# Kernel tuning notes

Hardware: AMD Instinct MI355X
Metric: run time of the kernel (lower is better)

The kernel has to match this reference:

```python
import jax, jax.numpy as jnp
import numpy as np

B = 128      # trees per batch
D = 10       # tree depth (perfect binary tree)
L = 2 ** D   # leaves per tree
V = 50000    # vocab
E = 300      # embed size
C = 5        # num classes


def setup_inputs() -> dict:
    key = jax.random.key(0)
    k0, k1, k2, k3 = jax.random.split(key, 4)
    return {
        "word_ids": jax.random.randint(k0, (B, L), 0, V),
        "embedding": jax.random.normal(k1, (V, E), jnp.float32) * 0.02,
        "W_w": jax.random.normal(k2, (E, 2 * E), jnp.float32) * (1.0 / np.sqrt(2 * E)),
        "W_b": jnp.zeros((E,), jnp.float32),
        "P_w": jax.random.normal(k3, (C, E), jnp.float32) * (1.0 / np.sqrt(E)),
        "P_b": jnp.zeros((C,), jnp.float32),
    }


def reference(word_ids, embedding, W_w, W_b, P_w, P_b):
    # Leaf nodes: relu(Embedding(word))  -> [B, L, E]
    h = jax.nn.relu(embedding[word_ids])
    # projection of every node (torch Linear: x @ W.T + b)
    logits = [jnp.einsum("bne,ce->bnc", h, P_w) + P_b]
    # Combine same-depth sibling pairs level by level (D fixed levels).
    for _ in range(D):
        pair = jnp.concatenate([h[:, 0::2], h[:, 1::2]], axis=-1)  # [B, n/2, 2E]
        h = jax.nn.relu(jnp.einsum("bnf,ef->bne", pair, W_w) + W_b)  # [B, n/2, E]
        logits.append(jnp.einsum("bne,ce->bnc", h, P_w) + P_b)
    # All node logits, leaves first then each internal level up to the root.
    return jnp.concatenate(logits, axis=1)  # [B, 2L-1, C]
```

## Files before the change

kernel.cpp:

```cpp
#include <hip/hip_runtime.h>
#include <hip/hip_bf16.h>

#define B_ 128
#define D_ 10
#define L_ 1024
#define E_ 300
#define C_ 5
#define NODES 2047
#define HSTR 304
#define KP 608
#define NP 320
#define PK 320
#define LSTR 328

typedef __attribute__((ext_vector_type(8))) short short8;
typedef __attribute__((ext_vector_type(4))) float f32x4;
typedef __hip_bfloat16 bf16;

__device__ __forceinline__ short f2bs(float v) {
  bf16 b = (bf16)v;
  return *reinterpret_cast<short*>(&b);
}

__device__ __forceinline__ short8 pack_relu(f32x4 v0, f32x4 v1) {
  short8 s;
#pragma unroll
  for (int j = 0; j < 4; j++) s[j] = f2bs(fmaxf(v0[j], 0.f));
#pragma unroll
  for (int j = 0; j < 4; j++) s[4 + j] = f2bs(fmaxf(v1[j], 0.f));
  return s;
}

__global__ __launch_bounds__(256) void prep_k(
    const float* __restrict__ emb, const float* __restrict__ Ww,
    const float* __restrict__ Pw, bf16* __restrict__ T, bf16* __restrict__ Wp,
    bf16* __restrict__ Pp, bf16* __restrict__ Pq, int V) {
  int idx = blockIdx.x * 256 + threadIdx.x;
  int tchunks = V * 38;
  if (idx < tchunks) {
    int v = idx / 38, c = idx % 38;
    const float* src = emb + (size_t)v * E_ + c * 8;
    f32x4 v0 = *(const f32x4*)src;
    f32x4 v1;
    if (c == 37) v1 = (f32x4){0.f, 0.f, 0.f, 0.f};
    else v1 = *(const f32x4*)(src + 4);
    *(short8*)(T + (size_t)v * HSTR + c * 8) = pack_relu(v0, v1);
  }
  if (idx < NP * KP) {
    int r = idx / KP, c = idx % KP;
    float v = 0.f;
    if (r < E_) {
      if (c < E_) v = Ww[r * 600 + c];
      else if (c >= HSTR && c < HSTR + E_) v = Ww[r * 600 + (c - 4)];
    }
    Wp[idx] = (bf16)v;
  }
  if (idx < 16 * PK) {
    int r = idx / PK, c = idx % PK;
    float v = (r < C_ && c < E_) ? Pw[r * E_ + c] : 0.f;
    Pp[idx] = (bf16)v;
  }
  if (idx < 2 * 16 * KP) {
    int p = idx / (16 * KP);
    int rem = idx % (16 * KP);
    int r = rem / KP, c = rem % KP;
    int e = c - p * HSTR;
    float v = (r < C_ && e >= 0 && e < E_) ? Pw[r * E_ + e] : 0.f;
    Pq[idx] = (bf16)v;
  }
}

__global__ __launch_bounds__(256) void fused_l1_k(
    const int* __restrict__ wid, const bf16* __restrict__ T,
    const bf16* __restrict__ Wp, const float* __restrict__ Wb,
    const bf16* __restrict__ Pq, const bf16* __restrict__ Pp,
    const float* __restrict__ Pb, bf16* __restrict__ h1,
    float* __restrict__ out) {
  __shared__ bf16 hs[64][LSTR];
  int tid = threadIdx.x;
  int w = tid >> 6, l = tid & 63, q = l & 15, half = l >> 4;
  int m0 = blockIdx.x * 64;

  int off0[4], off1[4];
#pragma unroll
  for (int rt = 0; rt < 4; rt++) {
    int mrow = m0 + rt * 16 + q;
    off0[rt] = wid[2 * mrow] * HSTR;
    off1[rt] = wid[2 * mrow + 1] * HSTR;
  }
  int lm = m0 + w * 16 + q;
  int lb0 = wid[2 * lm] * HSTR;
  int lb1 = wid[2 * lm + 1] * HSTR;

  f32x4 acc[4][5];
#pragma unroll
  for (int rt = 0; rt < 4; rt++)
#pragma unroll
    for (int nt = 0; nt < 5; nt++) acc[rt][nt] = (f32x4){0.f, 0.f, 0.f, 0.f};
  f32x4 pacc[2];
  pacc[0] = pacc[1] = (f32x4){0.f, 0.f, 0.f, 0.f};

  for (int ks = 0; ks < 19; ks++) {
    int k0 = ks * 32 + half * 8;
    int sel = k0 >= HSTR;
    int e0 = sel ? k0 - HSTR : k0;
    short8 a[4];
#pragma unroll
    for (int rt = 0; rt < 4; rt++)
      a[rt] = *(const short8*)(T + (sel ? off1[rt] : off0[rt]) + e0);
    short8 al = *(const short8*)(T + (sel ? lb1 : lb0) + e0);
    short8 pq0 = *(const short8*)(Pq + (size_t)q * KP + k0);
    short8 pq1 = *(const short8*)(Pq + (size_t)(16 + q) * KP + k0);
    pacc[0] = __builtin_amdgcn_mfma_f32_16x16x32_bf16(al, pq0, pacc[0], 0, 0, 0);
    pacc[1] = __builtin_amdgcn_mfma_f32_16x16x32_bf16(al, pq1, pacc[1], 0, 0, 0);
#pragma unroll
    for (int nt = 0; nt < 5; nt++) {
      short8 b =
          *(const short8*)(Wp + (size_t)(w * 80 + nt * 16 + q) * KP + k0);
#pragma unroll
      for (int rt = 0; rt < 4; rt++)
        acc[rt][nt] = __builtin_amdgcn_mfma_f32_16x16x32_bf16(a[rt], b,
                                                              acc[rt][nt], 0,
                                                              0, 0);
    }
  }

#pragma unroll
  for (int nt = 0; nt < 5; nt++) {
    int n = w * 80 + nt * 16 + q;
    float wb = (n < E_) ? Wb[n] : 0.f;
#pragma unroll
    for (int rt = 0; rt < 4; rt++)
#pragma unroll
      for (int j = 0; j < 4; j++) {
        int rl = rt * 16 + half * 4 + j;
        hs[rl][n] = (bf16)fmaxf(acc[rt][nt][j] + wb, 0.f);
      }
  }
  if (q < C_) {
    float pb = Pb[q];
#pragma unroll
    for (int p = 0; p < 2; p++)
#pragma unroll
      for (int j = 0; j < 4; j++) {
        int leaf = 2 * (m0 + w * 16 + half * 4 + j) + p;
        out[((size_t)(leaf >> 10) * NODES + (leaf & 1023)) * C_ + q] =
            pacc[p][j] + pb;
      }
  }
  __syncthreads();

  for (int i = tid; i < 64 * 38; i += 256) {
    int r = i / 38, c = i % 38;
    *(short8*)(h1 + (size_t)(m0 + r) * HSTR + c * 8) =
        *(const short8*)&hs[r][c * 8];
  }
  f32x4 pc = (f32x4){0.f, 0.f, 0.f, 0.f};
#pragma unroll
  for (int ks = 0; ks < 10; ks++) {
    int k0 = ks * 32 + half * 8;
    short8 a = *(const short8*)&hs[16 * w + q][k0];
    short8 b = *(const short8*)(Pp + (size_t)q * PK + k0);
    pc = __builtin_amdgcn_mfma_f32_16x16x32_bf16(a, b, pc, 0, 0, 0);
  }
  if (q < C_) {
    float pb = Pb[q];
#pragma unroll
    for (int j = 0; j < 4; j++) {
      int m = m0 + w * 16 + half * 4 + j;
      out[((size_t)(m >> 9) * NODES + 1024 + (m & 511)) * C_ + q] = pc[j] + pb;
    }
  }
}

__global__ __launch_bounds__(256) void combine_mfma_k(
    const bf16* __restrict__ h_in, const bf16* __restrict__ Wp,
    const float* __restrict__ Wb, const bf16* __restrict__ Pp,
    const float* __restrict__ Pb, bf16* __restrict__ h_out,
    float* __restrict__ out, int node_off, int nshift) {
  __shared__ bf16 hs[64][LSTR];
  int tid = threadIdx.x;
  int w = tid >> 6;
  int l = tid & 63;
  int q = l & 15;
  int half = l >> 4;
  size_t m0 = (size_t)blockIdx.x * 64;

  f32x4 acc[4][5];
#pragma unroll
  for (int rt = 0; rt < 4; rt++)
#pragma unroll
    for (int nt = 0; nt < 5; nt++) acc[rt][nt] = (f32x4){0.f, 0.f, 0.f, 0.f};

#pragma unroll 2
  for (int ks = 0; ks < 19; ks++) {
    int k0 = ks * 32 + half * 8;
    short8 a[4], b[5];
#pragma unroll
    for (int rt = 0; rt < 4; rt++)
      a[rt] = *(const short8*)(h_in + (m0 + rt * 16 + q) * KP + k0);
#pragma unroll
    for (int nt = 0; nt < 5; nt++)
      b[nt] = *(const short8*)(Wp + (size_t)(w * 80 + nt * 16 + q) * KP + k0);
#pragma unroll
    for (int rt = 0; rt < 4; rt++)
#pragma unroll
      for (int nt = 0; nt < 5; nt++)
        acc[rt][nt] = __builtin_amdgcn_mfma_f32_16x16x32_bf16(
            a[rt], b[nt], acc[rt][nt], 0, 0, 0);
  }

  float wb[5];
#pragma unroll
  for (int nt = 0; nt < 5; nt++) {
    int n = w * 80 + nt * 16 + q;
    wb[nt] = (n < E_) ? Wb[n] : 0.f;
  }
#pragma unroll
  for (int rt = 0; rt < 4; rt++)
#pragma unroll
    for (int nt = 0; nt < 5; nt++) {
      int n = w * 80 + nt * 16 + q;
#pragma unroll
      for (int j = 0; j < 4; j++) {
        int rl = rt * 16 + half * 4 + j;
        hs[rl][n] = (bf16)fmaxf(acc[rt][nt][j] + wb[nt], 0.f);
      }
    }
  __syncthreads();

  for (int i = tid; i < 64 * 38; i += 256) {
    int r = i / 38, c = i % 38;
    *(short8*)(h_out + (m0 + r) * HSTR + c * 8) = *(const short8*)&hs[r][c * 8];
  }

  f32x4 pacc = (f32x4){0.f, 0.f, 0.f, 0.f};
#pragma unroll
  for (int ks = 0; ks < 10; ks++) {
    short8 a = *(const short8*)(&hs[16 * w + q][ks * 32 + half * 8]);
    short8 b = *(const short8*)(Pp + (size_t)q * PK + ks * 32 + half * 8);
    pacc = __builtin_amdgcn_mfma_f32_16x16x32_bf16(a, b, pacc, 0, 0, 0);
  }
  if (q < C_) {
    float pb = Pb[q];
#pragma unroll
    for (int j = 0; j < 4; j++) {
      size_t m = m0 + w * 16 + half * 4 + j;
      size_t b_ = m >> nshift;
      size_t n = m & (((size_t)1 << nshift) - 1);
      out[((size_t)b_ * NODES + node_off + n) * C_ + q] = pacc[j] + pb;
    }
  }
}

__global__ __launch_bounds__(256) void tail_k(
    const bf16* __restrict__ h5, const bf16* __restrict__ Wp,
    const float* __restrict__ Wb, const bf16* __restrict__ Pp,
    const float* __restrict__ Pb, float* __restrict__ out) {
  __shared__ bf16 bufs[2][32][LSTR];
  int tid = threadIdx.x, b = blockIdx.x;
  int w = tid >> 6, l = tid & 63, q = l & 15, half = l >> 4;

  for (int i = tid; i < 32 * 38; i += 256) {
    int r = i / 38, c = i % 38;
    *(short8*)&bufs[0][r][c * 8] =
        *(const short8*)(h5 + ((size_t)b * 32 + r) * HSTR + c * 8);
  }
  __syncthreads();

  int p = 0, off = 2016, Mo = 16;
  for (int lev = 0; lev < 5; lev++) {
    f32x4 acc[5];
#pragma unroll
    for (int t = 0; t < 5; t++) acc[t] = (f32x4){0.f, 0.f, 0.f, 0.f};
    for (int ks = 0; ks < 19; ks++) {
      int k0 = ks * 32 + half * 8;
      int sel = k0 >= HSTR;
      int e0 = k0 - (sel ? HSTR : 0);
      short8 a = *(const short8*)&bufs[p][2 * q + sel][e0];
#pragma unroll
      for (int t = 0; t < 5; t++) {
        int nt = w + 4 * t;
        short8 bfr = *(const short8*)(Wp + ((size_t)nt * 16 + q) * KP + k0);
        acc[t] =
            __builtin_amdgcn_mfma_f32_16x16x32_bf16(a, bfr, acc[t], 0, 0, 0);
      }
    }
    __syncthreads();
#pragma unroll
    for (int t = 0; t < 5; t++) {
      int nt = w + 4 * t;
      int n = nt * 16 + q;
      float wb = (n < E_) ? Wb[n] : 0.f;
#pragma unroll
      for (int j = 0; j < 4; j++) {
        int r = half * 4 + j;
        bufs[p ^ 1][r][n] = (bf16)fmaxf(acc[t][j] + wb, 0.f);
      }
    }
    __syncthreads();
    if (w == 0) {
      f32x4 pc = (f32x4){0.f, 0.f, 0.f, 0.f};
#pragma unroll
      for (int ks = 0; ks < 10; ks++) {
        int k0 = ks * 32 + half * 8;
        short8 a = *(const short8*)&bufs[p ^ 1][q][k0];
        short8 bfr = *(const short8*)(Pp + (size_t)q * PK + k0);
        pc = __builtin_amdgcn_mfma_f32_16x16x32_bf16(a, bfr, pc, 0, 0, 0);
      }
      if (q < C_) {
        float pb = Pb[q];
#pragma unroll
        for (int j = 0; j < 4; j++) {
          int r = half * 4 + j;
          if (r < Mo) out[((size_t)b * NODES + off + r) * C_ + q] = pc[j] + pb;
        }
      }
    }
    p ^= 1;
    off += Mo;
    Mo >>= 1;
  }
}

extern "C" void kernel_launch(void* const* d_in, const int* in_sizes, int n_in,
                              void* d_out, int out_size, void* d_ws,
                              size_t ws_size, hipStream_t stream) {
  const int* wid = (const int*)d_in[0];
  const float* emb = (const float*)d_in[1];
  const float* Ww = (const float*)d_in[2];
  const float* Wb = (const float*)d_in[3];
  const float* Pw = (const float*)d_in[4];
  const float* Pb = (const float*)d_in[5];
  float* out = (float*)d_out;
  int V = in_sizes[1] / E_;

  bf16* hA = (bf16*)d_ws;
  bf16* hB = hA + (size_t)B_ * 512 * HSTR;
  bf16* Wp = hB + (size_t)B_ * 256 * HSTR;
  bf16* Pp = Wp + (size_t)NP * KP;
  bf16* Pq = Pp + (size_t)16 * PK;
  bf16* T = Pq + (size_t)2 * 16 * KP;

  int tchunks = V * 38;
  prep_k<<<(tchunks + 255) / 256, 256, 0, stream>>>(emb, Ww, Pw, T, Wp, Pp, Pq,
                                                    V);
  fused_l1_k<<<(B_ * 512) / 64, 256, 0, stream>>>(wid, T, Wp, Wb, Pq, Pp, Pb,
                                                  hA, out);
  bf16* cur = hA;
  int node_off = 1536;
  for (int lev = 2; lev <= 5; lev++) {
    int n_half = L_ >> lev;
    int M = B_ * n_half;
    bf16* nxt = (lev & 1) ? hA : hB;
    combine_mfma_k<<<M / 64, 256, 0, stream>>>(cur, Wp, Wb, Pp, Pb, nxt, out,
                                               node_off, D_ - lev);
    node_off += n_half;
    cur = nxt;
  }
  tail_k<<<B_, 256, 0, stream>>>(cur, Wp, Wb, Pp, Pb, out);
}
```

Measured before the change: 211.4 us.

## Shrink row tiles per block, add occupancy bounds and software-pipelined gather loads

Each block in the level-1 and combine kernels now covers fewer rows (32 or 16 instead of 64), so more blocks launch for the small later levels. LDS use shrinks and launch bounds request 4 blocks per CU, aiming at higher occupancy. The level-1 embedding gather is prefetched two k-steps ahead to hide load latency. The leaf projection is split across waves, and the tail of the projection K loop is zero-masked. In exchange, each W tile is reused across fewer rows, so there is more global/L2 traffic per output and a risk of register spills.

```diff
diff --git a/kernel.cpp b/kernel.cpp
--- a/kernel.cpp
+++ b/kernel.cpp
@@ -70,185 +70,193 @@
   }
 }
 
-__global__ __launch_bounds__(256) void fused_l1_k(
+#define PROJ_A(rowptr, ks, k0)                                        \
+  ((ks) == 9 && half >= 2 ? (short8){0, 0, 0, 0, 0, 0, 0, 0}          \
+                          : *(const short8*)((rowptr) + (k0)))
+
+__global__ __launch_bounds__(256, 4) void fused_l1_k(
     const int* __restrict__ wid, const bf16* __restrict__ T,
     const bf16* __restrict__ Wp, const float* __restrict__ Wb,
     const bf16* __restrict__ Pq, const bf16* __restrict__ Pp,
     const float* __restrict__ Pb, bf16* __restrict__ h1,
     float* __restrict__ out) {
-  __shared__ bf16 hs[64][LSTR];
+  __shared__ bf16 hs[33][HSTR];
   int tid = threadIdx.x;
   int w = tid >> 6, l = tid & 63, q = l & 15, half = l >> 4;
-  int m0 = blockIdx.x * 64;
-
-  int off0[4], off1[4];
-#pragma unroll
-  for (int rt = 0; rt < 4; rt++) {
-    int mrow = m0 + rt * 16 + q;
-    off0[rt] = wid[2 * mrow] * HSTR;
-    off1[rt] = wid[2 * mrow + 1] * HSTR;
-  }
-  int lm = m0 + w * 16 + q;
-  int lb0 = wid[2 * lm] * HSTR;
-  int lb1 = wid[2 * lm + 1] * HSTR;
-
-  f32x4 acc[4][5];
-#pragma unroll
-  for (int rt = 0; rt < 4; rt++)
+  int m0 = blockIdx.x * 32;
+
+  int mr0 = m0 + q, mr1 = m0 + 16 + q;
+  int o0a = wid[2 * mr0] * HSTR, o0b = wid[2 * mr0 + 1] * HSTR;
+  int o1a = wid[2 * mr1] * HSTR, o1b = wid[2 * mr1 + 1] * HSTR;
+
+  int p = w & 1, rtl = w >> 1;
+
+  f32x4 acc[2][5];
+#pragma unroll
+  for (int rt = 0; rt < 2; rt++)
 #pragma unroll
     for (int nt = 0; nt < 5; nt++) acc[rt][nt] = (f32x4){0.f, 0.f, 0.f, 0.f};
-  f32x4 pacc[2];
-  pacc[0] = pacc[1] = (f32x4){0.f, 0.f, 0.f, 0.f};
+  f32x4 pacc = (f32x4){0.f, 0.f, 0.f, 0.f};
+
+#define LDA(ks, d0, d1)                                          \
+  {                                                              \
+    int k0_ = (ks) * 32 + half * 8;                              \
+    int sel_ = k0_ >= HSTR;                                      \
+    int e0_ = sel_ ? k0_ - HSTR : k0_;                           \
+    d0 = *(const short8*)(T + (sel_ ? o0b : o0a) + e0_);         \
+    d1 = *(const short8*)(T + (sel_ ? o1b : o1a) + e0_);         \
+  }
+
+  short8 aA0, aA1, aB0, aB1, aC0, aC1;
+  LDA(0, aA0, aA1);
+  LDA(1, aB0, aB1);
 
   for (int ks = 0; ks < 19; ks++) {
+    int kn = ks + 2 <= 18 ? ks + 2 : 18;
+    LDA(kn, aC0, aC1);
     int k0 = ks * 32 + half * 8;
-    int sel = k0 >= HSTR;
-    int e0 = sel ? k0 - HSTR : k0;
-    short8 a[4];
-#pragma unroll
-    for (int rt = 0; rt < 4; rt++)
-      a[rt] = *(const short8*)(T + (sel ? off1[rt] : off0[rt]) + e0);
-    short8 al = *(const short8*)(T + (sel ? lb1 : lb0) + e0);
-    short8 pq0 = *(const short8*)(Pq + (size_t)q * KP + k0);
-    short8 pq1 = *(const short8*)(Pq + (size_t)(16 + q) * KP + k0);
-    pacc[0] = __builtin_amdgcn_mfma_f32_16x16x32_bf16(al, pq0, pacc[0], 0, 0, 0);
-    pacc[1] = __builtin_amdgcn_mfma_f32_16x16x32_bf16(al, pq1, pacc[1], 0, 0, 0);
+    short8 al = rtl ? aA1 : aA0;
+    short8 pqf = *(const short8*)(Pq + ((size_t)p * 16 + q) * KP + k0);
+    pacc = __builtin_amdgcn_mfma_f32_16x16x32_bf16(al, pqf, pacc, 0, 0, 0);
 #pragma unroll
     for (int nt = 0; nt < 5; nt++) {
       short8 b =
           *(const short8*)(Wp + (size_t)(w * 80 + nt * 16 + q) * KP + k0);
-#pragma unroll
-      for (int rt = 0; rt < 4; rt++)
-        acc[rt][nt] = __builtin_amdgcn_mfma_f32_16x16x32_bf16(a[rt], b,
-                                                              acc[rt][nt], 0,
-                                                              0, 0);
-    }
-  }
+      acc[0][nt] =
+          __builtin_amdgcn_mfma_f32_16x16x32_bf16(aA0, b, acc[0][nt], 0, 0, 0);
+      acc[1][nt] =
+          __builtin_amdgcn_mfma_f32_16x16x32_bf16(aA1, b, acc[1][nt], 0, 0, 0);
+    }
+    aA0 = aB0; aA1 = aB1;
+    aB0 = aC0; aB1 = aC1;
+  }
+#undef LDA
 
 #pragma unroll
   for (int nt = 0; nt < 5; nt++) {
     int n = w * 80 + nt * 16 + q;
     float wb = (n < E_) ? Wb[n] : 0.f;
-#pragma unroll
-    for (int rt = 0; rt < 4; rt++)
-#pragma unroll
-      for (int j = 0; j < 4; j++) {
-        int rl = rt * 16 + half * 4 + j;
-        hs[rl][n] = (bf16)fmaxf(acc[rt][nt][j] + wb, 0.f);
-      }
+    if (n < HSTR) {
+#pragma unroll
+      for (int rt = 0; rt < 2; rt++)
+#pragma unroll
+        for (int j = 0; j < 4; j++) {
+          int rl = rt * 16 + half * 4 + j;
+          hs[rl][n] = (bf16)fmaxf(acc[rt][nt][j] + wb, 0.f);
+        }
+    }
   }
   if (q < C_) {
     float pb = Pb[q];
 #pragma unroll
-    for (int p = 0; p < 2; p++)
-#pragma unroll
-      for (int j = 0; j < 4; j++) {
-        int leaf = 2 * (m0 + w * 16 + half * 4 + j) + p;
-        out[((size_t)(leaf >> 10) * NODES + (leaf & 1023)) * C_ + q] =
-            pacc[p][j] + pb;
-      }
+    for (int j = 0; j < 4; j++) {
+      int leaf = 2 * (m0 + rtl * 16 + half * 4 + j) + p;
+      out[((size_t)(leaf >> 10) * NODES + (leaf & 1023)) * C_ + q] =
+          pacc[j] + pb;
+    }
   }
   __syncthreads();
 
-  for (int i = tid; i < 64 * 38; i += 256) {
+  for (int i = tid; i < 32 * 38; i += 256) {
     int r = i / 38, c = i % 38;
     *(short8*)(h1 + (size_t)(m0 + r) * HSTR + c * 8) =
         *(const short8*)&hs[r][c * 8];
   }
-  f32x4 pc = (f32x4){0.f, 0.f, 0.f, 0.f};
-#pragma unroll
-  for (int ks = 0; ks < 10; ks++) {
-    int k0 = ks * 32 + half * 8;
-    short8 a = *(const short8*)&hs[16 * w + q][k0];
-    short8 b = *(const short8*)(Pp + (size_t)q * PK + k0);
-    pc = __builtin_amdgcn_mfma_f32_16x16x32_bf16(a, b, pc, 0, 0, 0);
-  }
-  if (q < C_) {
-    float pb = Pb[q];
-#pragma unroll
-    for (int j = 0; j < 4; j++) {
-      int m = m0 + w * 16 + half * 4 + j;
-      out[((size_t)(m >> 9) * NODES + 1024 + (m & 511)) * C_ + q] = pc[j] + pb;
-    }
-  }
-}
-
-__global__ __launch_bounds__(256) void combine_mfma_k(
+  if (w < 2) {
+    f32x4 pc = (f32x4){0.f, 0.f, 0.f, 0.f};
+#pragma unroll
+    for (int ks = 0; ks < 10; ks++) {
+      int k0 = ks * 32 + half * 8;
+      short8 a = PROJ_A(&hs[w * 16 + q][0], ks, k0);
+      short8 b = *(const short8*)(Pp + (size_t)q * PK + k0);
+      pc = __builtin_amdgcn_mfma_f32_16x16x32_bf16(a, b, pc, 0, 0, 0);
+    }
+    if (q < C_) {
+      float pb = Pb[q];
+#pragma unroll
+      for (int j = 0; j < 4; j++) {
+        int m = m0 + w * 16 + half * 4 + j;
+        out[((size_t)(m >> 9) * NODES + 1024 + (m & 511)) * C_ + q] =
+            pc[j] + pb;
+      }
+    }
+  }
+}
+
+template <int RT>
+__global__ __launch_bounds__(256, 4) void combine_k(
     const bf16* __restrict__ h_in, const bf16* __restrict__ Wp,
     const float* __restrict__ Wb, const bf16* __restrict__ Pp,
     const float* __restrict__ Pb, bf16* __restrict__ h_out,
     float* __restrict__ out, int node_off, int nshift) {
-  __shared__ bf16 hs[64][LSTR];
+  __shared__ bf16 hs[RT * 16 + 1][HSTR];
   int tid = threadIdx.x;
-  int w = tid >> 6;
-  int l = tid & 63;
-  int q = l & 15;
-  int half = l >> 4;
-  size_t m0 = (size_t)blockIdx.x * 64;
-
-  f32x4 acc[4][5];
-#pragma unroll
-  for (int rt = 0; rt < 4; rt++)
+  int w = tid >> 6, l = tid & 63, q = l & 15, half = l >> 4;
+  size_t m0 = (size_t)blockIdx.x * (RT * 16);
+
+  f32x4 acc[RT][5];
+#pragma unroll
+  for (int rt = 0; rt < RT; rt++)
 #pragma unroll
     for (int nt = 0; nt < 5; nt++) acc[rt][nt] = (f32x4){0.f, 0.f, 0.f, 0.f};
 
-#pragma unroll 2
   for (int ks = 0; ks < 19; ks++) {
     int k0 = ks * 32 + half * 8;
-    short8 a[4], b[5];
-#pragma unroll
-    for (int rt = 0; rt < 4; rt++)
+    short8 a[RT];
+#pragma unroll
+    for (int rt = 0; rt < RT; rt++)
       a[rt] = *(const short8*)(h_in + (m0 + rt * 16 + q) * KP + k0);
 #pragma unroll
-    for (int nt = 0; nt < 5; nt++)
-      b[nt] = *(const short8*)(Wp + (size_t)(w * 80 + nt * 16 + q) * KP + k0);
-#pragma unroll
-    for (int rt = 0; rt < 4; rt++)
-#pragma unroll
-      for (int nt = 0; nt < 5; nt++)
-        acc[rt][nt] = __builtin_amdgcn_mfma_f32_16x16x32_bf16(
-            a[rt], b[nt], acc[rt][nt], 0, 0, 0);
-  }
-
-  float wb[5];
+    for (int nt = 0; nt < 5; nt++) {
+      short8 b =
+          *(const short8*)(Wp + (size_t)(w * 80 + nt * 16 + q) * KP + k0);
+#pragma unroll
+      for (int rt = 0; rt < RT; rt++)
+        acc[rt][nt] = __builtin_amdgcn_mfma_f32_16x16x32_bf16(a[rt], b,
+                                                              acc[rt][nt], 0,
+                                                              0, 0);
+    }
+  }
+
 #pragma unroll
   for (int nt = 0; nt < 5; nt++) {
     int n = w * 80 + nt * 16 + q;
-    wb[nt] = (n < E_) ? Wb[n] : 0.f;
-  }
-#pragma unroll
-  for (int rt = 0; rt < 4; rt++)
-#pragma unroll
-    for (int nt = 0; nt < 5; nt++) {
-      int n = w * 80 + nt * 16 + q;
-#pragma unroll
-      for (int j = 0; j < 4; j++) {
-        int rl = rt * 16 + half * 4 + j;
-        hs[rl][n] = (bf16)fmaxf(acc[rt][nt][j] + wb[nt], 0.f);
-      }
-    }
+    float wb = (n < E_) ? Wb[n] : 0.f;
+    if (n < HSTR) {
+#pragma unroll
+      for (int rt = 0; rt < RT; rt++)
+#pragma unroll
+        for (int j = 0; j < 4; j++) {
+          int rl = rt * 16 + half * 4 + j;
+          hs[rl][n] = (bf16)fmaxf(acc[rt][nt][j] + wb, 0.f);
+        }
+    }
+  }
   __syncthreads();
 
-  for (int i = tid; i < 64 * 38; i += 256) {
+  for (int i = tid; i < RT * 16 * 38; i += 256) {
     int r = i / 38, c = i % 38;
     *(short8*)(h_out + (m0 + r) * HSTR + c * 8) = *(const short8*)&hs[r][c * 8];
   }
 
-  f32x4 pacc = (f32x4){0.f, 0.f, 0.f, 0.f};
-#pragma unroll
-  for (int ks = 0; ks < 10; ks++) {
-    short8 a = *(const short8*)(&hs[16 * w + q][ks * 32 + half * 8]);
-    short8 b = *(const short8*)(Pp + (size_t)q * PK + ks * 32 + half * 8);
-    pacc = __builtin_amdgcn_mfma_f32_16x16x32_bf16(a, b, pacc, 0, 0, 0);
-  }
-  if (q < C_) {
-    float pb = Pb[q];
-#pragma unroll
-    for (int j = 0; j < 4; j++) {
-      size_t m = m0 + w * 16 + half * 4 + j;
-      size_t b_ = m >> nshift;
-      size_t n = m & (((size_t)1 << nshift) - 1);
-      out[((size_t)b_ * NODES + node_off + n) * C_ + q] = pacc[j] + pb;
+  if (w < RT) {
+    f32x4 pacc = (f32x4){0.f, 0.f, 0.f, 0.f};
+#pragma unroll
+    for (int ks = 0; ks < 10; ks++) {
+      int k0 = ks * 32 + half * 8;
+      short8 a = PROJ_A(&hs[16 * w + q][0], ks, k0);
+      short8 b = *(const short8*)(Pp + (size_t)q * PK + k0);
+      pacc = __builtin_amdgcn_mfma_f32_16x16x32_bf16(a, b, pacc, 0, 0, 0);
+    }
+    if (q < C_) {
+      float pb = Pb[q];
+#pragma unroll
+      for (int j = 0; j < 4; j++) {
+        size_t m = m0 + w * 16 + half * 4 + j;
+        size_t b_ = m >> nshift;
+        size_t n = m & (((size_t)1 << nshift) - 1);
+        out[((size_t)b_ * NODES + node_off + n) * C_ + q] = pacc[j] + pb;
+      }
     }
   }
 }
@@ -345,18 +353,11 @@
   int tchunks = V * 38;
   prep_k<<<(tchunks + 255) / 256, 256, 0, stream>>>(emb, Ww, Pw, T, Wp, Pp, Pq,
                                                     V);
-  fused_l1_k<<<(B_ * 512) / 64, 256, 0, stream>>>(wid, T, Wp, Wb, Pq, Pp, Pb,
+  fused_l1_k<<<(B_ * 512) / 32, 256, 0, stream>>>(wid, T, Wp, Wb, Pq, Pp, Pb,
                                                   hA, out);
-  bf16* cur = hA;
-  int node_off = 1536;
-  for (int lev = 2; lev <= 5; lev++) {
-    int n_half = L_ >> lev;
-    int M = B_ * n_half;
-    bf16* nxt = (lev & 1) ? hA : hB;
-    combine_mfma_k<<<M / 64, 256, 0, stream>>>(cur, Wp, Wb, Pp, Pb, nxt, out,
-                                               node_off, D_ - lev);
-    node_off += n_half;
-    cur = nxt;
-  }
-  tail_k<<<B_, 256, 0, stream>>>(cur, Wp, Wb, Pp, Pb, out);
-}
+  combine_k<2><<<1024, 256, 0, stream>>>(hA, Wp, Wb, Pp, Pb, hB, out, 1536, 8);
+  combine_k<2><<<512, 256, 0, stream>>>(hB, Wp, Wb, Pp, Pb, hA, out, 1792, 7);
+  combine_k<1><<<512, 256, 0, stream>>>(hA, Wp, Wb, Pp, Pb, hB, out, 1920, 6);
+  combine_k<1><<<256, 256, 0, stream>>>(hB, Wp, Wb, Pp, Pb, hA, out, 1984, 5);
+  tail_k<<<B_, 256, 0, stream>>>(hA, Wp, Wb, Pp, Pb, out);
+}
```

Result: slower. 238.9 us (+13.0%).
